# Kernel optimization log

Hardware: AMD Instinct MI355X
Metric: run time of the kernel (lower is better)

The kernel has to match this reference:

```python
import jax, jax.numpy as jnp
import numpy as np

B, T, D, H = 2, 2048, 1024, 16
DK = D // H


def setup_inputs() -> dict:
    key = jax.random.key(0)
    ks = jax.random.split(key, 9)
    s = 1.0 / np.sqrt(D)
    x = jax.random.normal(ks[0], (B, T, D), dtype=jnp.float32)
    # causal mask (1 = attend, 0 = masked), broadcast over batch and heads
    mask = jnp.tril(jnp.ones((T, T), dtype=jnp.int32))[None, None, :, :]
    Wq = jax.random.uniform(ks[1], (D, D), jnp.float32, -s, s)
    bq = jax.random.uniform(ks[2], (D,), jnp.float32, -s, s)
    Wk = jax.random.uniform(ks[3], (D, D), jnp.float32, -s, s)
    bk = jax.random.uniform(ks[4], (D,), jnp.float32, -s, s)
    Wv = jax.random.uniform(ks[5], (D, D), jnp.float32, -s, s)
    bv = jax.random.uniform(ks[6], (D,), jnp.float32, -s, s)
    Wo = jax.random.uniform(ks[7], (D, D), jnp.float32, -s, s)
    bo = jax.random.uniform(ks[8], (D,), jnp.float32, -s, s)
    return {"x": x, "mask": mask, "Wq": Wq, "bq": bq, "Wk": Wk, "bk": bk,
            "Wv": Wv, "bv": bv, "Wo": Wo, "bo": bo}


def reference(x, mask, Wq, bq, Wk, bk, Wv, bv, Wo, bo):
    # nn.Linear: y = x @ W.T + b
    q = (x @ Wq.T + bq).reshape(B, T, H, DK).transpose(0, 2, 1, 3)  # [B,H,T,DK]
    k = (x @ Wk.T + bk).reshape(B, T, H, DK).transpose(0, 2, 1, 3)
    v = (x @ Wv.T + bv).reshape(B, T, H, DK).transpose(0, 2, 1, 3)
    scores = jnp.einsum('bhqd,bhkd->bhqk', q, k) / np.sqrt(DK).astype(np.float32)
    scores = jnp.where(mask == 0, -jnp.inf, scores)
    attn = jax.nn.softmax(scores, axis=-1)
    out = jnp.einsum('bhqk,bhkd->bhqd', attn, v)  # [B,H,T,DK]
    out = out.transpose(0, 2, 1, 3).reshape(B, T, D)
    return out @ Wo.T + bo
```

## Files before the change

kernel.cpp:

```cpp
#include <hip/hip_runtime.h>

typedef unsigned short u16;
typedef unsigned int u32;
typedef unsigned long long u64;
typedef __attribute__((ext_vector_type(8))) short short8;
typedef __attribute__((ext_vector_type(4))) float f32x4;

#define B_ 2
#define T_ 2048
#define H_ 16
#define DK_ 64
#define QSCALE 0.18033688011112042f

__device__ __forceinline__ u16 f2bf(float f){
  unsigned u = __float_as_uint(f);
  return (u16)((u + 0x7fffu + ((u >> 16) & 1u)) >> 16);
}

__device__ __forceinline__ u32 cvtpk(float lo, float hi){
  u32 r;
  asm("v_cvt_pk_bf16_f32 %0, %1, %2" : "=v"(r) : "v"(lo), "v"(hi));
  return r;
}

#define EXP2(x) __builtin_exp2f(x)

#if defined(__has_builtin)
#if __has_builtin(__builtin_amdgcn_global_load_lds)
#define HAS_GLLDS 1
#endif
#endif

#ifdef HAS_GLLDS
__device__ __forceinline__ void gl_lds16(const u16* g, u16* l){
  __builtin_amdgcn_global_load_lds(
      (__attribute__((address_space(1))) void*)(void*)g,
      (__attribute__((address_space(3))) void*)(void*)l, 16, 0, 0);
}
__device__ __forceinline__ void wait_vm4(){ asm volatile("s_waitcnt vmcnt(4)" ::: "memory"); }
__device__ __forceinline__ void wait_vm0(){ asm volatile("s_waitcnt vmcnt(0)" ::: "memory"); }
__device__ __forceinline__ void pipe_bar(){
  asm volatile("" ::: "memory");
  __builtin_amdgcn_s_barrier();
  asm volatile("" ::: "memory");
}
#else
__device__ __forceinline__ void wait_vm4(){}
__device__ __forceinline__ void wait_vm0(){}
__device__ __forceinline__ void pipe_bar(){ __syncthreads(); }
#endif

__global__ __launch_bounds__(256) void conv_all(
    const float* __restrict__ x, const float* __restrict__ wq, const float* __restrict__ wk,
    const float* __restrict__ wv, const float* __restrict__ wo,
    u16* __restrict__ xb, u16* __restrict__ wqb, u16* __restrict__ wkb,
    u16* __restrict__ wvb, u16* __restrict__ wob)
{
  int gid = blockIdx.x * 256 + threadIdx.x;
  const float* src; u16* dst; int off;
  if (gid < 1048576){ src = x; dst = xb; off = gid; }
  else {
    int t = gid - 1048576; int s = t >> 18; off = t & 262143;
    src = (s==0)?wq:((s==1)?wk:((s==2)?wv:wo));
    dst = (s==0)?wqb:((s==1)?wkb:((s==2)?wvb:wob));
  }
  float4 v = ((const float4*)src)[off];
  u64 r = (u64)f2bf(v.x) | ((u64)f2bf(v.y)<<16) | ((u64)f2bf(v.z)<<32) | ((u64)f2bf(v.w)<<48);
  ((u64*)dst)[off] = r;
}

template<int QKV>
__global__ __launch_bounds__(256, 3) void gemm_k5(
    const u16* __restrict__ A,
    const u16* __restrict__ W0, const u16* __restrict__ W1, const u16* __restrict__ W2,
    const float* __restrict__ b0, const float* __restrict__ b1, const float* __restrict__ b2,
    void* __restrict__ o0, void* __restrict__ o1, void* __restrict__ o2)
{
  __shared__ u16 As[3 * 4096];
  __shared__ u16 Bs[3 * 4096];
  const int tid = threadIdx.x;
  const int sel = QKV ? (blockIdx.x >> 3) : 0;
  const int n0 = (blockIdx.x & 7) * 128;
  const int m0 = blockIdx.y * 128;
  const u16* Bw = (sel==0)?W0:((sel==1)?W1:W2);
  const float* bias = (sel==0)?b0:((sel==1)?b1:b2);
  const int w = tid>>6, l = tid&63;
  const int lr = l&15, lg = l>>4;
  const int wm = (w&1)*64, wn = (w>>1)*64;
  const u16* Ab = A  + (size_t)m0*1024 + (size_t)(l>>2)*1024 + (l&3)*8;
  const u16* Bb = Bw + (size_t)n0*1024 + (size_t)(l>>2)*1024 + (l&3)*8;
  f32x4 acc[4][4] = {};

  auto STAGE = [&](int t, int pb){
#pragma unroll
    for (int i = 0; i < 2; ++i){
      int c = w*2 + i;
#ifdef HAS_GLLDS
      gl_lds16(Ab + (size_t)(16*c)*1024 + t*32, &As[pb*4096 + c*512]);
      gl_lds16(Bb + (size_t)(16*c)*1024 + t*32, &Bs[pb*4096 + c*512]);
#else
      *(uint4*)&As[pb*4096 + c*512 + l*8] = *(const uint4*)(Ab + (size_t)(16*c)*1024 + t*32);
      *(uint4*)&Bs[pb*4096 + c*512 + l*8] = *(const uint4*)(Bb + (size_t)(16*c)*1024 + t*32);
#endif
    }
  };

  STAGE(0, 0); STAGE(1, 1);
  wait_vm4();
  pipe_bar();
  for (int it = 0; it < 32; ++it){
    const int pb = it % 3;
    if (it < 30) STAGE(it + 2, (it + 2) % 3);
    short8 af[4], bf[4];
#pragma unroll
    for (int mi=0;mi<4;++mi) af[mi] = *(const short8*)&As[pb*4096 + (wm+16*mi+lr)*32 + 8*lg];
#pragma unroll
    for (int ni=0;ni<4;++ni) bf[ni] = *(const short8*)&Bs[pb*4096 + (wn+16*ni+lr)*32 + 8*lg];
#pragma unroll
    for (int mi=0;mi<4;++mi)
#pragma unroll
      for (int ni=0;ni<4;++ni)
        acc[mi][ni] = __builtin_amdgcn_mfma_f32_16x16x32_bf16(af[mi], bf[ni], acc[mi][ni], 0,0,0);
    if (it < 31){
      if (it < 30) wait_vm4();
      else         wait_vm0();
      pipe_bar();
    }
  }

  float bv[4];
#pragma unroll
  for (int ni=0;ni<4;++ni) bv[ni] = bias[n0+wn+16*ni+lr];
  void* C = QKV ? ((sel==0)?o0:((sel==1)?o1:o2)) : o0;
#pragma unroll
  for (int mi=0;mi<4;++mi)
#pragma unroll
    for (int r=0;r<4;++r){
      const int trow = m0 + wm + 16*mi + 4*lg + r;
#pragma unroll
      for (int ni=0;ni<4;++ni){
        float v = acc[mi][ni][r] + bv[ni];
        int n = n0 + wn + 16*ni + lr;
        if (!QKV){
          ((float*)C)[(size_t)trow*1024 + n] = v;
        } else if (sel == 0){
          ((u16*)C)[(size_t)trow*1024 + n] = f2bf(v * QSCALE);
        } else if (sel == 1){
          int nsw = (n & ~63) | ((n & 63) ^ ((trow & 7) << 3));
          ((u16*)C)[(size_t)trow*1024 + nsw] = f2bf(v);
        } else {
          ((u16*)C)[(size_t)trow*1024 + n] = f2bf(v);
        }
      }
    }
}

__global__ __launch_bounds__(256) void transpose_v_k(const u16* __restrict__ V,
                                                     u16* __restrict__ VT){
  __shared__ u16 L[64 * 72];
  const int tid = threadIdx.x;
  const int tc = blockIdx.x, h = blockIdx.y, b = blockIdx.z;
#pragma unroll
  for (int p = 0; p < 2; ++p){
    int row = (tid >> 3) + 32 * p, g = tid & 7;
    *(uint4*)&L[row * 72 + g * 8] =
        *(const uint4*)(V + ((size_t)(b * T_ + tc * 64 + row) * H_ + h) * DK_ + g * 8);
  }
  __syncthreads();
#pragma unroll
  for (int p = 0; p < 2; ++p){
    int d = tid >> 2, g8 = (tid & 3) + 4 * p;
    union { uint4 u; u16 s[8]; } tv;
#pragma unroll
    for (int i = 0; i < 8; ++i){
      int pp = 8 * g8 + i;
      int tl = 16 * (pp & 3) + (pp >> 2);
      tv.s[i] = L[tl * 72 + d];
    }
    *(uint4*)(VT + ((size_t)(b * H_ + h) * DK_ + d) * T_ + tc * 64 + ((8 * g8) ^ ((d & 7) << 3))) = tv.u;
  }
}

__global__ __launch_bounds__(256, 2) void attn_v5(
    const u16* __restrict__ Q, const u16* __restrict__ K,
    const u16* __restrict__ VT, u16* __restrict__ O)
{
  __shared__ u16 Ks[3 * 4096];
  __shared__ u16 VTs[3 * 4096];
  __shared__ u16 Ps[4][32 * 72];
  const int tid = threadIdx.x;
  const int w = tid>>6, l = tid&63;
  const int lr = l&15, lg = l>>4;
  const int h = blockIdx.y, b = blockIdx.z;
  const int qtb = (b==0) ? blockIdx.x : (15 - blockIdx.x);
  const int q0 = qtb * 128;
  const int wrow0 = q0 + w*32;
  const int sl_r = l>>3, sl_c = (l&7)*8;
  const size_t kbase = ((size_t)(b*T_) * H_ + h) * DK_;
  const size_t vbase = (size_t)(b*H_ + h) * DK_ * (size_t)T_;

  auto STAGE = [&](int kt, int pb){
#pragma unroll
    for (int p=0;p<2;++p){
      int r0 = 8*w + 32*p;
#ifdef HAS_GLLDS
      gl_lds16(K  + kbase + (size_t)(kt*64 + r0 + sl_r)*1024 + sl_c, &Ks[pb*4096 + r0*64]);
      gl_lds16(VT + vbase + (size_t)(r0 + sl_r)*T_ + kt*64 + sl_c, &VTs[pb*4096 + r0*64]);
#else
      *(uint4*)&Ks[pb*4096 + (r0+sl_r)*64 + sl_c] =
          *(const uint4*)(K + kbase + (size_t)(kt*64 + r0 + sl_r)*1024 + sl_c);
      *(uint4*)&VTs[pb*4096 + (r0+sl_r)*64 + sl_c] =
          *(const uint4*)(VT + vbase + (size_t)(r0 + sl_r)*T_ + kt*64 + sl_c);
#endif
    }
  };

  short8 qf[2][2];
#pragma unroll
  for (int mi=0;mi<2;++mi)
#pragma unroll
    for (int s=0;s<2;++s)
      qf[mi][s] = *(const short8*)(Q + kbase + (size_t)(wrow0 + 16*mi + lr)*1024 + s*32 + 8*lg);

  f32x4 acc[2][4] = {};
  float lsum[2][4] = {};
  const int ktend = 2*qtb + 1;

  STAGE(0, 0); STAGE(1, 1);
  wait_vm4();
  pipe_bar();
  for (int kt = 0; kt <= ktend; ++kt){
    const int pb = kt % 3;
    const bool more2 = (kt + 2 <= ktend);
    if (more2) STAGE(kt + 2, (kt + 2) % 3);
    if (kt*64 <= wrow0 + 31){
      short8 kf[4][2];
#pragma unroll
      for (int j0=0;j0<4;++j0)
#pragma unroll
        for (int s=0;s<2;++s)
          kf[j0][s] = *(const short8*)&Ks[pb*4096 + (j0*16+lr)*64 + (((4*s+lg) ^ (lr&7))<<3)];
      f32x4 sc[2][4];
#pragma unroll
      for (int mi=0;mi<2;++mi)
#pragma unroll
        for (int j0=0;j0<4;++j0){
          f32x4 z = {};
          z = __builtin_amdgcn_mfma_f32_16x16x32_bf16(qf[mi][0], kf[j0][0], z, 0,0,0);
          z = __builtin_amdgcn_mfma_f32_16x16x32_bf16(qf[mi][1], kf[j0][1], z, 0,0,0);
          sc[mi][j0] = z;
        }
      const bool diag = (kt*64 + 63 > wrow0);
#pragma unroll
      for (int mi=0;mi<2;++mi)
#pragma unroll
        for (int r=0;r<4;++r){
          float p0,p1,p2,p3;
          if (diag){
            const int lim = wrow0 + 16*mi + 4*lg + r - kt*64;
            p0 = (lr      <= lim) ? EXP2(sc[mi][0][r]) : 0.f;
            p1 = (16+lr   <= lim) ? EXP2(sc[mi][1][r]) : 0.f;
            p2 = (32+lr   <= lim) ? EXP2(sc[mi][2][r]) : 0.f;
            p3 = (48+lr   <= lim) ? EXP2(sc[mi][3][r]) : 0.f;
          } else {
            p0 = EXP2(sc[mi][0][r]); p1 = EXP2(sc[mi][1][r]);
            p2 = EXP2(sc[mi][2][r]); p3 = EXP2(sc[mi][3][r]);
          }
          lsum[mi][r] += (p0+p1)+(p2+p3);
          u64 pv = (u64)cvtpk(p0,p1) | ((u64)cvtpk(p2,p3) << 32);
          *(u64*)&Ps[w][(16*mi+4*lg+r)*72 + 4*lr] = pv;
        }
#pragma unroll
      for (int ks=0;ks<2;++ks){
        short8 pf0 = *(const short8*)&Ps[w][lr*72      + 32*ks + 8*lg];
        short8 pf1 = *(const short8*)&Ps[w][(16+lr)*72 + 32*ks + 8*lg];
#pragma unroll
        for (int d0=0;d0<4;++d0){
          short8 vf = *(const short8*)&VTs[pb*4096 + (d0*16+lr)*64 + (((4*ks+lg) ^ (lr&7))<<3)];
          acc[0][d0] = __builtin_amdgcn_mfma_f32_16x16x32_bf16(pf0, vf, acc[0][d0], 0,0,0);
          acc[1][d0] = __builtin_amdgcn_mfma_f32_16x16x32_bf16(pf1, vf, acc[1][d0], 0,0,0);
        }
      }
    }
    if (kt < ktend){
      if (more2) wait_vm4();
      else       wait_vm0();
      pipe_bar();
    }
  }

#pragma unroll
  for (int mi=0;mi<2;++mi)
#pragma unroll
    for (int r=0;r<4;++r){
      float v = lsum[mi][r];
      v += __shfl_xor(v,1); v += __shfl_xor(v,2);
      v += __shfl_xor(v,4); v += __shfl_xor(v,8);
      lsum[mi][r] = 1.0f / v;
    }
#pragma unroll
  for (int mi=0;mi<2;++mi)
#pragma unroll
    for (int d0=0;d0<4;++d0)
#pragma unroll
      for (int r=0;r<4;++r){
        float ov = acc[mi][d0][r] * lsum[mi][r];
        O[kbase + (size_t)(wrow0 + 16*mi + 4*lg + r)*1024 + d0*16 + lr] = f2bf(ov);
      }
}

extern "C" void kernel_launch(void* const* d_in, const int* in_sizes, int n_in,
                              void* d_out, int out_size, void* d_ws, size_t ws_size,
                              hipStream_t stream)
{
  const float* x  = (const float*)d_in[0];
  const float* Wq = (const float*)d_in[2];
  const float* bq = (const float*)d_in[3];
  const float* Wk = (const float*)d_in[4];
  const float* bk = (const float*)d_in[5];
  const float* Wv = (const float*)d_in[6];
  const float* bv = (const float*)d_in[7];
  const float* Wo = (const float*)d_in[8];
  const float* bo = (const float*)d_in[9];

  char* ws = (char*)d_ws;
  u16* xb  = (u16*)(ws + 0);
  u16* wqb = (u16*)(ws + 8388608);
  u16* wkb = (u16*)(ws + 10485760);
  u16* wvb = (u16*)(ws + 12582912);
  u16* wob = (u16*)(ws + 14680064);
  u16* qb  = (u16*)(ws + 16777216);
  u16* kb  = (u16*)(ws + 25165824);
  u16* vb  = (u16*)(ws + 33554432);
  u16* vtb = xb;
  u16* ab  = vb;

  conv_all<<<8192, 256, 0, stream>>>(x, Wq, Wk, Wv, Wo, xb, wqb, wkb, wvb, wob);

  gemm_k5<1><<<dim3(24, 32), 256, 0, stream>>>(
      xb, wqb, wkb, wvb, bq, bk, bv, (void*)qb, (void*)kb, (void*)vb);

  transpose_v_k<<<dim3(T_/64, H_, B_), 256, 0, stream>>>(vb, vtb);

  attn_v5<<<dim3(T_/128, H_, B_), 256, 0, stream>>>(qb, kb, vtb, ab);

  gemm_k5<0><<<dim3(8, 32), 256, 0, stream>>>(
      ab, wob, wob, wob, bo, bo, bo, d_out, d_out, d_out);
}
```

Measured before the change: 137.3 us.

## Compute S^T so softmax probabilities feed PV MFMA directly from registers

Swaps the MFMA operand order so each lane holds a column slice of the transposed scores. The bf16-packed probabilities can then be used directly as the A operand of the PV MFMA, removing the per-wave LDS round trip for P. The V transpose permutation is changed to match the new key ordering. The K/V pipeline drops from triple to double buffering with plain __syncthreads, which frees LDS for 3 blocks per CU, at the cost of less prefetch depth and a full barrier every tile.

New measurement: 133.8 us. 2.5% less time.

```diff
diff --git a/kernel.cpp b/kernel.cpp
--- a/kernel.cpp
+++ b/kernel.cpp
@@ -21,6 +21,13 @@
   u32 r;
   asm("v_cvt_pk_bf16_f32 %0, %1, %2" : "=v"(r) : "v"(lo), "v"(hi));
   return r;
+}
+
+__device__ __forceinline__ short8 pack8(const f32x4 a, const f32x4 b){
+  union { u32 u[4]; short8 s; } t;
+  t.u[0] = cvtpk(a[0], a[1]); t.u[1] = cvtpk(a[2], a[3]);
+  t.u[2] = cvtpk(b[0], b[1]); t.u[3] = cvtpk(b[2], b[3]);
+  return t.s;
 }
 
 #define EXP2(x) __builtin_exp2f(x)
@@ -174,139 +181,123 @@
 #pragma unroll
     for (int i = 0; i < 8; ++i){
       int pp = 8 * g8 + i;
-      int tl = 16 * (pp & 3) + (pp >> 2);
+      int tl = 16 * (2 * ((pp >> 5) & 1) + ((pp >> 2) & 1)) + 4 * ((pp >> 3) & 3) + (pp & 3);
       tv.s[i] = L[tl * 72 + d];
     }
     *(uint4*)(VT + ((size_t)(b * H_ + h) * DK_ + d) * T_ + tc * 64 + ((8 * g8) ^ ((d & 7) << 3))) = tv.u;
   }
 }
 
-__global__ __launch_bounds__(256, 2) void attn_v5(
+__global__ __launch_bounds__(256, 3) void attn_v6(
     const u16* __restrict__ Q, const u16* __restrict__ K,
     const u16* __restrict__ VT, u16* __restrict__ O)
 {
-  __shared__ u16 Ks[3 * 4096];
-  __shared__ u16 VTs[3 * 4096];
-  __shared__ u16 Ps[4][32 * 72];
+  __shared__ u16 Ks[2][64 * 64];
+  __shared__ u16 VTs[2][64 * 64];
   const int tid = threadIdx.x;
-  const int w = tid>>6, l = tid&63;
-  const int lr = l&15, lg = l>>4;
+  const int w = tid >> 6, l = tid & 63;
+  const int lr = l & 15, lg = l >> 4;
   const int h = blockIdx.y, b = blockIdx.z;
-  const int qtb = (b==0) ? blockIdx.x : (15 - blockIdx.x);
+  const int qtb = (b == 0) ? blockIdx.x : (15 - blockIdx.x);
   const int q0 = qtb * 128;
-  const int wrow0 = q0 + w*32;
-  const int sl_r = l>>3, sl_c = (l&7)*8;
-  const size_t kbase = ((size_t)(b*T_) * H_ + h) * DK_;
-  const size_t vbase = (size_t)(b*H_ + h) * DK_ * (size_t)T_;
+  const int wrow0 = q0 + w * 32;
+  const int sl_r = l >> 3, sl_c = (l & 7) * 8;
+  const size_t kbase = ((size_t)(b * T_) * H_ + h) * DK_;
+  const size_t vbase = (size_t)(b * H_ + h) * DK_ * (size_t)T_;
 
   auto STAGE = [&](int kt, int pb){
 #pragma unroll
-    for (int p=0;p<2;++p){
-      int r0 = 8*w + 32*p;
+    for (int p = 0; p < 2; ++p){
+      int r0 = 8 * w + 32 * p;
 #ifdef HAS_GLLDS
-      gl_lds16(K  + kbase + (size_t)(kt*64 + r0 + sl_r)*1024 + sl_c, &Ks[pb*4096 + r0*64]);
-      gl_lds16(VT + vbase + (size_t)(r0 + sl_r)*T_ + kt*64 + sl_c, &VTs[pb*4096 + r0*64]);
+      gl_lds16(K  + kbase + (size_t)(kt * 64 + r0 + sl_r) * 1024 + sl_c, &Ks[pb][r0 * 64]);
+      gl_lds16(VT + vbase + (size_t)(r0 + sl_r) * T_ + kt * 64 + sl_c, &VTs[pb][r0 * 64]);
 #else
-      *(uint4*)&Ks[pb*4096 + (r0+sl_r)*64 + sl_c] =
-          *(const uint4*)(K + kbase + (size_t)(kt*64 + r0 + sl_r)*1024 + sl_c);
-      *(uint4*)&VTs[pb*4096 + (r0+sl_r)*64 + sl_c] =
-          *(const uint4*)(VT + vbase + (size_t)(r0 + sl_r)*T_ + kt*64 + sl_c);
+      *(uint4*)&Ks[pb][(r0 + sl_r) * 64 + sl_c] =
+          *(const uint4*)(K + kbase + (size_t)(kt * 64 + r0 + sl_r) * 1024 + sl_c);
+      *(uint4*)&VTs[pb][(r0 + sl_r) * 64 + sl_c] =
+          *(const uint4*)(VT + vbase + (size_t)(r0 + sl_r) * T_ + kt * 64 + sl_c);
 #endif
     }
   };
 
   short8 qf[2][2];
 #pragma unroll
-  for (int mi=0;mi<2;++mi)
-#pragma unroll
-    for (int s=0;s<2;++s)
-      qf[mi][s] = *(const short8*)(Q + kbase + (size_t)(wrow0 + 16*mi + lr)*1024 + s*32 + 8*lg);
+  for (int mi = 0; mi < 2; ++mi)
+#pragma unroll
+    for (int s = 0; s < 2; ++s)
+      qf[mi][s] = *(const short8*)(Q + kbase + (size_t)(wrow0 + 16 * mi + lr) * 1024 + s * 32 + 8 * lg);
 
   f32x4 acc[2][4] = {};
-  float lsum[2][4] = {};
-  const int ktend = 2*qtb + 1;
-
-  STAGE(0, 0); STAGE(1, 1);
-  wait_vm4();
-  pipe_bar();
+  float lsum[2] = {0.f, 0.f};
+  const int ktend = 2 * qtb + 1;
+
+  STAGE(0, 0);
+  __syncthreads();
   for (int kt = 0; kt <= ktend; ++kt){
-    const int pb = kt % 3;
-    const bool more2 = (kt + 2 <= ktend);
-    if (more2) STAGE(kt + 2, (kt + 2) % 3);
-    if (kt*64 <= wrow0 + 31){
+    const int pb = kt & 1;
+    if (kt < ktend) STAGE(kt + 1, pb ^ 1);
+    if (kt * 64 <= wrow0 + 31){
       short8 kf[4][2];
 #pragma unroll
-      for (int j0=0;j0<4;++j0)
-#pragma unroll
-        for (int s=0;s<2;++s)
-          kf[j0][s] = *(const short8*)&Ks[pb*4096 + (j0*16+lr)*64 + (((4*s+lg) ^ (lr&7))<<3)];
-      f32x4 sc[2][4];
-#pragma unroll
-      for (int mi=0;mi<2;++mi)
-#pragma unroll
-        for (int j0=0;j0<4;++j0){
+      for (int j0 = 0; j0 < 4; ++j0)
+#pragma unroll
+        for (int s = 0; s < 2; ++s)
+          kf[j0][s] = *(const short8*)&Ks[pb][(j0 * 16 + lr) * 64 + (((4 * s + lg) ^ (lr & 7)) << 3)];
+      short8 pf[2][2];
+      const bool diag = (kt * 64 + 63 > wrow0);
+      const int kc0 = kt * 64 + 4 * lg;
+#pragma unroll
+      for (int mi = 0; mi < 2; ++mi){
+        f32x4 pr[4];
+        float lacc = 0.f;
+        const int qrow = wrow0 + 16 * mi + lr;
+#pragma unroll
+        for (int j0 = 0; j0 < 4; ++j0){
           f32x4 z = {};
-          z = __builtin_amdgcn_mfma_f32_16x16x32_bf16(qf[mi][0], kf[j0][0], z, 0,0,0);
-          z = __builtin_amdgcn_mfma_f32_16x16x32_bf16(qf[mi][1], kf[j0][1], z, 0,0,0);
-          sc[mi][j0] = z;
+          z = __builtin_amdgcn_mfma_f32_16x16x32_bf16(kf[j0][0], qf[mi][0], z, 0, 0, 0);
+          z = __builtin_amdgcn_mfma_f32_16x16x32_bf16(kf[j0][1], qf[mi][1], z, 0, 0, 0);
+#pragma unroll
+          for (int r = 0; r < 4; ++r){
+            float e = EXP2(z[r]);
+            if (diag && (kc0 + 16 * j0 + r > qrow)) e = 0.f;
+            pr[j0][r] = e;
+            lacc += e;
+          }
         }
-      const bool diag = (kt*64 + 63 > wrow0);
-#pragma unroll
-      for (int mi=0;mi<2;++mi)
-#pragma unroll
-        for (int r=0;r<4;++r){
-          float p0,p1,p2,p3;
-          if (diag){
-            const int lim = wrow0 + 16*mi + 4*lg + r - kt*64;
-            p0 = (lr      <= lim) ? EXP2(sc[mi][0][r]) : 0.f;
-            p1 = (16+lr   <= lim) ? EXP2(sc[mi][1][r]) : 0.f;
-            p2 = (32+lr   <= lim) ? EXP2(sc[mi][2][r]) : 0.f;
-            p3 = (48+lr   <= lim) ? EXP2(sc[mi][3][r]) : 0.f;
-          } else {
-            p0 = EXP2(sc[mi][0][r]); p1 = EXP2(sc[mi][1][r]);
-            p2 = EXP2(sc[mi][2][r]); p3 = EXP2(sc[mi][3][r]);
-          }
-          lsum[mi][r] += (p0+p1)+(p2+p3);
-          u64 pv = (u64)cvtpk(p0,p1) | ((u64)cvtpk(p2,p3) << 32);
-          *(u64*)&Ps[w][(16*mi+4*lg+r)*72 + 4*lr] = pv;
+        lsum[mi] += lacc;
+        pf[mi][0] = pack8(pr[0], pr[1]);
+        pf[mi][1] = pack8(pr[2], pr[3]);
+      }
+#pragma unroll
+      for (int ks = 0; ks < 2; ++ks)
+#pragma unroll
+        for (int d0 = 0; d0 < 4; ++d0){
+          short8 vf = *(const short8*)&VTs[pb][(d0 * 16 + lr) * 64 + (((4 * ks + lg) ^ (lr & 7)) << 3)];
+          acc[0][d0] = __builtin_amdgcn_mfma_f32_16x16x32_bf16(pf[0][ks], vf, acc[0][d0], 0, 0, 0);
+          acc[1][d0] = __builtin_amdgcn_mfma_f32_16x16x32_bf16(pf[1][ks], vf, acc[1][d0], 0, 0, 0);
         }
-#pragma unroll
-      for (int ks=0;ks<2;++ks){
-        short8 pf0 = *(const short8*)&Ps[w][lr*72      + 32*ks + 8*lg];
-        short8 pf1 = *(const short8*)&Ps[w][(16+lr)*72 + 32*ks + 8*lg];
-#pragma unroll
-        for (int d0=0;d0<4;++d0){
-          short8 vf = *(const short8*)&VTs[pb*4096 + (d0*16+lr)*64 + (((4*ks+lg) ^ (lr&7))<<3)];
-          acc[0][d0] = __builtin_amdgcn_mfma_f32_16x16x32_bf16(pf0, vf, acc[0][d0], 0,0,0);
-          acc[1][d0] = __builtin_amdgcn_mfma_f32_16x16x32_bf16(pf1, vf, acc[1][d0], 0,0,0);
-        }
+    }
+    __syncthreads();
+  }
+
+#pragma unroll
+  for (int mi = 0; mi < 2; ++mi){
+    float v = lsum[mi];
+    v += __shfl_xor(v, 16);
+    v += __shfl_xor(v, 32);
+    float inv = 1.0f / v;
+    float invr[4];
+#pragma unroll
+    for (int r = 0; r < 4; ++r) invr[r] = __shfl(inv, 4 * lg + r);
+#pragma unroll
+    for (int d0 = 0; d0 < 4; ++d0)
+#pragma unroll
+      for (int r = 0; r < 4; ++r){
+        float ov = acc[mi][d0][r] * invr[r];
+        O[kbase + (size_t)(wrow0 + 16 * mi + 4 * lg + r) * 1024 + d0 * 16 + lr] = f2bf(ov);
       }
-    }
-    if (kt < ktend){
-      if (more2) wait_vm4();
-      else       wait_vm0();
-      pipe_bar();
-    }
-  }
-
-#pragma unroll
-  for (int mi=0;mi<2;++mi)
-#pragma unroll
-    for (int r=0;r<4;++r){
-      float v = lsum[mi][r];
-      v += __shfl_xor(v,1); v += __shfl_xor(v,2);
-      v += __shfl_xor(v,4); v += __shfl_xor(v,8);
-      lsum[mi][r] = 1.0f / v;
-    }
-#pragma unroll
-  for (int mi=0;mi<2;++mi)
-#pragma unroll
-    for (int d0=0;d0<4;++d0)
-#pragma unroll
-      for (int r=0;r<4;++r){
-        float ov = acc[mi][d0][r] * lsum[mi][r];
-        O[kbase + (size_t)(wrow0 + 16*mi + 4*lg + r)*1024 + d0*16 + lr] = f2bf(ov);
-      }
+  }
 }
 
 extern "C" void kernel_launch(void* const* d_in, const int* in_sizes, int n_in,
@@ -342,7 +333,7 @@
 
   transpose_v_k<<<dim3(T_/64, H_, B_), 256, 0, stream>>>(vb, vtb);
 
-  attn_v5<<<dim3(T_/128, H_, B_), 256, 0, stream>>>(qb, kb, vtb, ab);
+  attn_v6<<<dim3(T_/128, H_, B_), 256, 0, stream>>>(qb, kb, vtb, ab);
 
   gemm_k5<0><<<dim3(8, 32), 256, 0, stream>>>(
       ab, wob, wob, wob, bo, bo, bo, d_out, d_out, d_out);
```
